# Performance work log

Hardware: AMD Instinct MI355X
Metric: run time of the kernel (lower is better)

## Reference

```python
import jax, jax.numpy as jnp
import numpy as np

T = 4            # number of atom types (experts)
F = (32, 64, 128)  # filter_neuron
H = (256, 256, 256)  # fitting_neuron
AXIS = 16        # axis_neuron
B, N, S = 8, 512, 128  # frames, atoms, SEL_A_max
DESC = AXIS * F[2]     # 2048, fitting input dim


def setup_inputs() -> dict:
    key = jax.random.key(0)
    ks = jax.random.split(key, 18)

    def w(k, shape, fan_in):
        return jax.random.normal(k, shape, jnp.float32) / np.float32(np.sqrt(fan_in))

    def b(k, shape):
        return 0.01 * jax.random.normal(k, shape, jnp.float32)

    return {
        "sym_coord": jax.random.normal(ks[0], (B, N, S, 4), jnp.float32),
        "types": jax.random.randint(ks[1], (B, N), 0, T, jnp.int32),
        # per-type filter MLP: 1 -> 32 -> 64 -> 128, tanh
        "Wf0": w(ks[2], (T, F[0], 1), 1), "bf0": b(ks[3], (T, F[0])),
        "Wf1": w(ks[4], (T, F[1], F[0]), F[0]), "bf1": b(ks[5], (T, F[1])),
        "Wf2": w(ks[6], (T, F[2], F[1]), F[1]), "bf2": b(ks[7], (T, F[2])),
        # per-type fitting MLP: 2048 -> 256 -> 256 -> 256 -> 1
        "Wt0": w(ks[8], (T, H[0], DESC), DESC), "bt0": b(ks[9], (T, H[0])),
        "Wt1": w(ks[10], (T, H[1], H[0]), H[0]), "bt1": b(ks[11], (T, H[1])),
        "Wt2": w(ks[12], (T, H[2], H[1]), H[1]), "bt2": b(ks[13], (T, H[2])),
        "Wo": w(ks[14], (T, 1, H[2]), H[2]), "bo": b(ks[15], (T, 1)),
    }


def reference(sym_coord, types, Wf0, bf0, Wf1, bf1, Wf2, bf2,
              Wt0, bt0, Wt1, bt1, Wt2, bt2, Wo, bo):
    t = types  # [B,N] expert index per atom
    s = sym_coord[..., :1]  # radial channel, [B,N,S,1]
    # type-routed filter MLP, vectorized via per-atom weight gather
    G = jnp.tanh(jnp.einsum('bnsi,bnfi->bnsf', s, Wf0[t]) + bf0[t][:, :, None, :])
    G = jnp.tanh(jnp.einsum('bnsf,bngf->bnsg', G, Wf1[t]) + bf1[t][:, :, None, :])
    G = jnp.tanh(jnp.einsum('bnsg,bnmg->bnsm', G, Wf2[t]) + bf2[t][:, :, None, :])  # [B,N,S,128]
    # RG = R^T G : [B,N,4,128]
    RG = jnp.einsum('bnsd,bnsm->bndm', sym_coord, G)
    # GRRG = RG^T RG[:, :AXIS] : [B,N,128,AXIS]
    GRRG = jnp.einsum('bndm,bnda->bnma', RG, RG[..., :AXIS])
    D = GRRG.reshape(GRRG.shape[0], GRRG.shape[1], -1)  # [B,N,2048]
    # type-routed fitting MLP
    h = jnp.tanh(jnp.einsum('bnd,bnhd->bnh', D, Wt0[t]) + bt0[t])
    h = jnp.tanh(jnp.einsum('bnh,bngh->bng', h, Wt1[t]) + bt1[t])
    h = jnp.tanh(jnp.einsum('bng,bnhg->bnh', h, Wt2[t]) + bt2[t])
    E_atom = jnp.einsum('bnh,bnoh->bno', h, Wo[t])[..., 0] + bo[t][..., 0]  # [B,N]
    return E_atom.sum(axis=-1)  # per-frame energy, [B]
```

## Files before the change

kernel.cpp:

```cpp
#include <hip/hip_runtime.h>
#include <hip/hip_bf16.h>

#define NATOMS 4096
#define DESC_ 2048
#define MAXTILES 67

typedef short short8 __attribute__((ext_vector_type(8)));
typedef float f32x4 __attribute__((ext_vector_type(4)));
typedef unsigned short u16x8 __attribute__((ext_vector_type(8)));
typedef unsigned short u16x4 __attribute__((ext_vector_type(4)));
typedef unsigned short u16;

__device__ __forceinline__ float fast_tanh(float x) {
    float e = __expf(2.0f * x);
    return 1.0f - 2.0f * __builtin_amdgcn_rcpf(e + 1.0f);
}

__device__ __forceinline__ float bf2f(u16 h) {
    union { unsigned int u; float f; } v; v.u = ((unsigned int)h) << 16;
    return v.f;
}
__device__ __forceinline__ void f2bf_split(float x, u16& hi, u16& lo) {
    union { float f; unsigned int u; } v; v.f = x;
    unsigned int hb = v.u & 0xffff0000u;
    hi = (u16)(hb >> 16);
    union { unsigned int u; float f; } w; w.u = hb;
    union { float f; unsigned int u; } z; z.f = x - w.f;
    lo = (u16)(z.u >> 16);
}

__device__ __forceinline__ void conv4(const float* __restrict__ src,
                                      u16* __restrict__ dh, u16* __restrict__ dl,
                                      int idx)
{
    float4 v = *(const float4*)(src + idx);
    u16x4 oh, ol;
    u16 h, l;
    f2bf_split(v.x, h, l); oh[0] = h; ol[0] = l;
    f2bf_split(v.y, h, l); oh[1] = h; ol[1] = l;
    f2bf_split(v.z, h, l); oh[2] = h; ol[2] = l;
    f2bf_split(v.w, h, l); oh[3] = h; ol[3] = l;
    *(u16x4*)(dh + idx) = oh;
    *(u16x4*)(dl + idx) = ol;
}

__global__ __launch_bounds__(256) void prep_kernel(
    const int* __restrict__ types, int* __restrict__ perm, int* __restrict__ meta,
    const float* __restrict__ Wf1, u16* __restrict__ F1h, u16* __restrict__ F1l,
    const float* __restrict__ Wf2, u16* __restrict__ F2h, u16* __restrict__ F2l,
    const float* __restrict__ Wt0, u16* __restrict__ W0h, u16* __restrict__ W0l,
    const float* __restrict__ Wt1, u16* __restrict__ W1h, u16* __restrict__ W1l,
    const float* __restrict__ Wt2, u16* __restrict__ W2h, u16* __restrict__ W2l)
{
    __shared__ int cnt[256 * 4];
    __shared__ int tot[4];
    __shared__ int tstart[4];
    int b = blockIdx.x;
    int tid = threadIdx.x;
    if (b == 0) {
        int base = tid * 16;
        int c0 = 0, c1 = 0, c2 = 0, c3 = 0;
        for (int i = 0; i < 16; ++i) {
            int t = types[base + i];
            c0 += (t == 0); c1 += (t == 1); c2 += (t == 2); c3 += (t == 3);
        }
        cnt[tid * 4 + 0] = c0; cnt[tid * 4 + 1] = c1;
        cnt[tid * 4 + 2] = c2; cnt[tid * 4 + 3] = c3;
        __syncthreads();
        if (tid < 4) {
            int run = 0;
            for (int th = 0; th < 256; ++th) {
                int v = cnt[th * 4 + tid];
                cnt[th * 4 + tid] = run;
                run += v;
            }
            tot[tid] = run;
        }
        __syncthreads();
        if (tid == 0) {
            int run = 0, nt = 0;
            for (int t = 0; t < 4; ++t) { tstart[t] = run; run += tot[t]; }
            for (int t = 0; t < 4; ++t) {
                int cT = tot[t];
                for (int off = 0; off < cT; off += 64) {
                    meta[1 + nt * 3 + 0] = t;
                    meta[1 + nt * 3 + 1] = tstart[t] + off;
                    meta[1 + nt * 3 + 2] = (cT - off < 64) ? (cT - off) : 64;
                    nt++;
                }
            }
            meta[0] = nt;
        }
        __syncthreads();
        for (int i = 0; i < 16; ++i) {
            int idx = base + i;
            int t = types[idx];
            perm[tstart[t] + cnt[tid * 4 + t]++] = idx;
        }
        return;
    }
    b -= 1;
    const float* src; u16 *dh, *dl; int n, base;
    if (b < 2048)      { src = Wt0; dh = W0h; dl = W0l; n = 2097152; base = b; }
    else if (b < 2304) { src = Wt1; dh = W1h; dl = W1l; n = 262144;  base = b - 2048; }
    else if (b < 2560) { src = Wt2; dh = W2h; dl = W2l; n = 262144;  base = b - 2304; }
    else if (b < 2568) { src = Wf1; dh = F1h; dl = F1l; n = 8192;    base = b - 2560; }
    else               { src = Wf2; dh = F2h; dl = F2l; n = 32768;   base = b - 2568; }
    int idx = (base * 256 + tid) * 4;
    if (idx < n) conv4(src, dh, dl, idx);
}

__global__ __launch_bounds__(256) void filter_kernel(
    const float* __restrict__ sym, const int* __restrict__ types,
    const int* __restrict__ perm,
    const float* __restrict__ Wf0, const float* __restrict__ bf0,
    const u16* __restrict__ F1h, const u16* __restrict__ F1l,
    const float* __restrict__ bf1,
    const u16* __restrict__ F2h, const u16* __restrict__ F2l,
    const float* __restrict__ bf2,
    u16* __restrict__ Dh, u16* __restrict__ Dl)
{
    __shared__ char lds[40960] __attribute__((aligned(16)));
    float* Rl  = (float*)lds;
    u16*   G1h = (u16*)(lds + 2048);
    u16*   G1l = (u16*)(lds + 20480);
    float* RGl = (float*)(lds + 38912);

    int p = blockIdx.x;
    int tid = threadIdx.x;
    int atom = perm[p];
    int t = __builtin_amdgcn_readfirstlane(types[atom]);
    int lane = tid & 63;
    int wv   = tid >> 6;
    int kg   = lane >> 4;
    int l15  = lane & 15;

    ((float2*)Rl)[tid] = ((const float2*)(sym + (size_t)atom * 512))[tid];

    {
        const float4* w0p = (const float4*)(Wf0 + t * 32 + kg * 8);
        float4 w04 = w0p[0], w14 = w0p[1];
        const float4* b0p = (const float4*)(bf0 + t * 32 + kg * 8);
        float4 b04 = b0p[0], b14 = b0p[1];

        short8 ah[2], al[2];
        #pragma unroll
        for (int mi = 0; mi < 2; ++mi) {
            int s = (wv * 2 + mi) * 16 + l15;
            float sv = sym[(size_t)atom * 512 + s * 4];
            float g[8];
            g[0] = fast_tanh(sv * w04.x + b04.x);
            g[1] = fast_tanh(sv * w04.y + b04.y);
            g[2] = fast_tanh(sv * w04.z + b04.z);
            g[3] = fast_tanh(sv * w04.w + b04.w);
            g[4] = fast_tanh(sv * w14.x + b14.x);
            g[5] = fast_tanh(sv * w14.y + b14.y);
            g[6] = fast_tanh(sv * w14.z + b14.z);
            g[7] = fast_tanh(sv * w14.w + b14.w);
            #pragma unroll
            for (int j = 0; j < 8; ++j) {
                u16 h, l; f2bf_split(g[j], h, l);
                ah[mi][j] = (short)h; al[mi][j] = (short)l;
            }
        }

        short8 b1h[4], b1l[4];
        float  bias1[4];
        #pragma unroll
        for (int nt = 0; nt < 4; ++nt) {
            int off = t * 2048 + (nt * 16 + l15) * 32 + kg * 8;
            b1h[nt] = *(const short8*)(F1h + off);
            b1l[nt] = *(const short8*)(F1l + off);
            bias1[nt] = bf1[t * 64 + nt * 16 + l15];
        }
        #pragma unroll
        for (int mi = 0; mi < 2; ++mi) {
            int mt = wv * 2 + mi;
            #pragma unroll
            for (int nt = 0; nt < 4; ++nt) {
                f32x4 acc = {0.f, 0.f, 0.f, 0.f};
                acc = __builtin_amdgcn_mfma_f32_16x16x32_bf16(ah[mi], b1h[nt], acc, 0, 0, 0);
                acc = __builtin_amdgcn_mfma_f32_16x16x32_bf16(ah[mi], b1l[nt], acc, 0, 0, 0);
                acc = __builtin_amdgcn_mfma_f32_16x16x32_bf16(al[mi], b1h[nt], acc, 0, 0, 0);
                int rowb = mt * 16 + kg * 4;
                #pragma unroll
                for (int r = 0; r < 4; ++r) {
                    u16 h, l;
                    f2bf_split(fast_tanh(acc[r] + bias1[nt]), h, l);
                    G1h[(rowb + r) * 72 + nt * 16 + l15] = h;
                    G1l[(rowb + r) * 72 + nt * 16 + l15] = l;
                }
            }
        }
    }
    __syncthreads();

    {
        short8 b2h[2][2], b2l[2][2];
        float  bias2[2];
        #pragma unroll
        for (int ntl = 0; ntl < 2; ++ntl) {
            int nt = wv * 2 + ntl;
            bias2[ntl] = bf2[t * 128 + nt * 16 + l15];
            #pragma unroll
            for (int ks = 0; ks < 2; ++ks) {
                int off = t * 8192 + (nt * 16 + l15) * 64 + ks * 32 + kg * 8;
                b2h[ntl][ks] = *(const short8*)(F2h + off);
                b2l[ntl][ks] = *(const short8*)(F2l + off);
            }
        }
        float rg[4][2];
        #pragma unroll
        for (int d = 0; d < 4; ++d) { rg[d][0] = 0.f; rg[d][1] = 0.f; }

        #pragma unroll 2
        for (int mt = 0; mt < 8; ++mt) {
            int i0 = (mt * 16 + l15) * 72 + kg * 8;
            short8 a0h = *(const short8*)&G1h[i0];
            short8 a0l = *(const short8*)&G1l[i0];
            short8 a1h = *(const short8*)&G1h[i0 + 32];
            short8 a1l = *(const short8*)&G1l[i0 + 32];
            f32x4 acc0 = {0.f,0.f,0.f,0.f}, acc1 = {0.f,0.f,0.f,0.f};
            acc0 = __builtin_amdgcn_mfma_f32_16x16x32_bf16(a0h, b2h[0][0], acc0, 0,0,0);
            acc0 = __builtin_amdgcn_mfma_f32_16x16x32_bf16(a0h, b2l[0][0], acc0, 0,0,0);
            acc0 = __builtin_amdgcn_mfma_f32_16x16x32_bf16(a0l, b2h[0][0], acc0, 0,0,0);
            acc0 = __builtin_amdgcn_mfma_f32_16x16x32_bf16(a1h, b2h[0][1], acc0, 0,0,0);
            acc0 = __builtin_amdgcn_mfma_f32_16x16x32_bf16(a1h, b2l[0][1], acc0, 0,0,0);
            acc0 = __builtin_amdgcn_mfma_f32_16x16x32_bf16(a1l, b2h[0][1], acc0, 0,0,0);
            acc1 = __builtin_amdgcn_mfma_f32_16x16x32_bf16(a0h, b2h[1][0], acc1, 0,0,0);
            acc1 = __builtin_amdgcn_mfma_f32_16x16x32_bf16(a0h, b2l[1][0], acc1, 0,0,0);
            acc1 = __builtin_amdgcn_mfma_f32_16x16x32_bf16(a0l, b2h[1][0], acc1, 0,0,0);
            acc1 = __builtin_amdgcn_mfma_f32_16x16x32_bf16(a1h, b2h[1][1], acc1, 0,0,0);
            acc1 = __builtin_amdgcn_mfma_f32_16x16x32_bf16(a1h, b2l[1][1], acc1, 0,0,0);
            acc1 = __builtin_amdgcn_mfma_f32_16x16x32_bf16(a1l, b2h[1][1], acc1, 0,0,0);
            int rowb = mt * 16 + kg * 4;
            #pragma unroll
            for (int r = 0; r < 4; ++r) {
                float4 R4 = *(const float4*)&Rl[(rowb + r) * 4];
                float g0 = fast_tanh(acc0[r] + bias2[0]);
                float g1 = fast_tanh(acc1[r] + bias2[1]);
                rg[0][0] += R4.x * g0; rg[1][0] += R4.y * g0;
                rg[2][0] += R4.z * g0; rg[3][0] += R4.w * g0;
                rg[0][1] += R4.x * g1; rg[1][1] += R4.y * g1;
                rg[2][1] += R4.z * g1; rg[3][1] += R4.w * g1;
            }
        }
        #pragma unroll
        for (int off = 16; off < 64; off <<= 1) {
            #pragma unroll
            for (int d = 0; d < 4; ++d) {
                rg[d][0] += __shfl_xor(rg[d][0], off, 64);
                rg[d][1] += __shfl_xor(rg[d][1], off, 64);
            }
        }
        if (kg == 0) {
            #pragma unroll
            for (int d = 0; d < 4; ++d) {
                RGl[d * 128 + wv * 32 + l15]      = rg[d][0];
                RGl[d * 128 + wv * 32 + 16 + l15] = rg[d][1];
            }
        }
    }
    __syncthreads();

    {
        int m = tid >> 1;
        int ab = (tid & 1) * 8;
        float rm0 = RGl[0 * 128 + m], rm1 = RGl[1 * 128 + m];
        float rm2 = RGl[2 * 128 + m], rm3 = RGl[3 * 128 + m];
        u16x8 oh, ol;
        #pragma unroll
        for (int q = 0; q < 8; ++q) {
            int a = ab + q;
            float v = rm0 * RGl[0 * 128 + a] + rm1 * RGl[1 * 128 + a]
                    + rm2 * RGl[2 * 128 + a] + rm3 * RGl[3 * 128 + a];
            u16 h, l; f2bf_split(v, h, l);
            oh[q] = h; ol[q] = l;
        }
        size_t base = (size_t)p * DESC_ + m * 16 + ab;
        *(u16x8*)(Dh + base) = oh;
        *(u16x8*)(Dl + base) = ol;
    }
}

__global__ __launch_bounds__(256) void fit0_partial(
    const u16* __restrict__ inh, const u16* __restrict__ inl,
    const u16* __restrict__ Wh,  const u16* __restrict__ Wl,
    float* __restrict__ part, const int* __restrict__ meta)
{
    __shared__ char lds[18432] __attribute__((aligned(16)));
    u16* Ath = (u16*)lds;
    u16* Atl = (u16*)(lds + 9216);

    int ntiles = meta[0];
    int b = blockIdx.x;
    int tile = b >> 4;
    if (tile >= ntiles) return;
    int hq  = (b >> 2) & 3;
    int ksp = b & 3;
    int t   = __builtin_amdgcn_readfirstlane(meta[1 + tile * 3 + 0]);
    int p0  = meta[1 + tile * 3 + 1];
    int cnt = meta[1 + tile * 3 + 2];
    int h0b = hq * 64;

    int tid = threadIdx.x;
    int lane = tid & 63;
    int wv   = tid >> 6;
    int kg   = lane >> 4;
    int l15  = lane & 15;

    int srow = tid >> 2;
    int skc  = (tid & 3) * 16;
    int agrow = p0 + srow; if (agrow > NATOMS - 1) agrow = NATOMS - 1;
    const u16* arow_h = inh + (size_t)agrow * 2048;
    const u16* arow_l = inl + (size_t)agrow * 2048;
    int hmy = h0b + wv * 16 + l15;
    const u16* brow_h = Wh + ((size_t)t * 256 + hmy) * 2048;
    const u16* brow_l = Wl + ((size_t)t * 256 + hmy) * 2048;

    f32x4 acc[4];
    #pragma unroll
    for (int mt = 0; mt < 4; ++mt) acc[mt] = (f32x4){0.f, 0.f, 0.f, 0.f};

    int kbase = ksp * 512;
    for (int k0 = kbase; k0 < kbase + 512; k0 += 64) {
        u16x8 a0 = *(const u16x8*)(arow_h + k0 + skc);
        u16x8 a1 = *(const u16x8*)(arow_h + k0 + skc + 8);
        u16x8 a2 = *(const u16x8*)(arow_l + k0 + skc);
        u16x8 a3 = *(const u16x8*)(arow_l + k0 + skc + 8);
        __syncthreads();
        int si = srow * 72 + skc;
        *(u16x8*)&Ath[si]     = a0;
        *(u16x8*)&Ath[si + 8] = a1;
        *(u16x8*)&Atl[si]     = a2;
        *(u16x8*)&Atl[si + 8] = a3;
        __syncthreads();

        #pragma unroll
        for (int ks = 0; ks < 2; ++ks) {
            short8 bh = *(const short8*)(brow_h + k0 + ks * 32 + kg * 8);
            short8 bl = *(const short8*)(brow_l + k0 + ks * 32 + kg * 8);
            #pragma unroll
            for (int mt = 0; mt < 4; ++mt) {
                int ai = (mt * 16 + l15) * 72 + ks * 32 + kg * 8;
                short8 ah = *(const short8*)&Ath[ai];
                short8 al = *(const short8*)&Atl[ai];
                acc[mt] = __builtin_amdgcn_mfma_f32_16x16x32_bf16(ah, bh, acc[mt], 0, 0, 0);
                acc[mt] = __builtin_amdgcn_mfma_f32_16x16x32_bf16(ah, bl, acc[mt], 0, 0, 0);
                acc[mt] = __builtin_amdgcn_mfma_f32_16x16x32_bf16(al, bh, acc[mt], 0, 0, 0);
            }
        }
    }

    float* pdst = part + (size_t)ksp * (NATOMS * 256);
    #pragma unroll
    for (int mt = 0; mt < 4; ++mt) {
        #pragma unroll
        for (int r = 0; r < 4; ++r) {
            int al = mt * 16 + kg * 4 + r;
            if (al < cnt)
                pdst[(size_t)(p0 + al) * 256 + hmy] = acc[mt][r];
        }
    }
}

__global__ __launch_bounds__(256) void fit0_epi(
    const float* __restrict__ part, const float* __restrict__ bias,
    const int* __restrict__ perm, const int* __restrict__ types,
    u16* __restrict__ outh, u16* __restrict__ outl)
{
    const int PN = NATOMS * 256;
    int idx = (blockIdx.x * 256 + threadIdx.x) * 4;
    if (idx >= PN) return;
    int p = idx >> 8;
    int t = types[perm[p]];
    float4 s0 = *(const float4*)(part + idx);
    float4 s1 = *(const float4*)(part + PN + idx);
    float4 s2 = *(const float4*)(part + 2 * PN + idx);
    float4 s3 = *(const float4*)(part + 3 * PN + idx);
    float4 bv = *(const float4*)(bias + t * 256 + (idx & 255));
    float v0 = fast_tanh(s0.x + s1.x + s2.x + s3.x + bv.x);
    float v1 = fast_tanh(s0.y + s1.y + s2.y + s3.y + bv.y);
    float v2 = fast_tanh(s0.z + s1.z + s2.z + s3.z + bv.z);
    float v3 = fast_tanh(s0.w + s1.w + s2.w + s3.w + bv.w);
    u16x4 oh, ol; u16 h, l;
    f2bf_split(v0, h, l); oh[0] = h; ol[0] = l;
    f2bf_split(v1, h, l); oh[1] = h; ol[1] = l;
    f2bf_split(v2, h, l); oh[2] = h; ol[2] = l;
    f2bf_split(v3, h, l); oh[3] = h; ol[3] = l;
    *(u16x4*)(outh + idx) = oh;
    *(u16x4*)(outl + idx) = ol;
}

__global__ __launch_bounds__(256) void fit_mfma(
    const u16* __restrict__ inh, const u16* __restrict__ inl,
    const u16* __restrict__ Wh,  const u16* __restrict__ Wl,
    const float* __restrict__ bias,
    u16* __restrict__ outh, u16* __restrict__ outl,
    int K, const int* __restrict__ meta)
{
    __shared__ char lds[36864] __attribute__((aligned(16)));
    u16* Ath = (u16*)lds;
    u16* Atl = (u16*)(lds + 9216);
    u16* Bth = (u16*)(lds + 18432);
    u16* Btl = (u16*)(lds + 27648);

    int ntiles = meta[0];
    int tile = blockIdx.x >> 2;
    if (tile >= ntiles) return;
    int hq  = blockIdx.x & 3;
    int t   = __builtin_amdgcn_readfirstlane(meta[1 + tile * 3 + 0]);
    int p0  = meta[1 + tile * 3 + 1];
    int cnt = meta[1 + tile * 3 + 2];
    int h0b = hq * 64;

    int tid = threadIdx.x;
    int lane = tid & 63;
    int wv   = tid >> 6;
    int kg   = lane >> 4;
    int l15  = lane & 15;

    int srow = tid >> 2;
    int skc  = (tid & 3) * 16;
    int agrow = p0 + srow; if (agrow > NATOMS - 1) agrow = NATOMS - 1;
    const u16* arow_h = inh + (size_t)agrow * K;
    const u16* arow_l = inl + (size_t)agrow * K;
    const u16* brow_h = Wh + ((size_t)t * 256 + h0b + srow) * K;
    const u16* brow_l = Wl + ((size_t)t * 256 + h0b + srow) * K;

    f32x4 acc[4];
    #pragma unroll
    for (int mt = 0; mt < 4; ++mt) acc[mt] = (f32x4){0.f, 0.f, 0.f, 0.f};

    for (int k0 = 0; k0 < K; k0 += 64) {
        u16x8 a0 = *(const u16x8*)(arow_h + k0 + skc);
        u16x8 a1 = *(const u16x8*)(arow_h + k0 + skc + 8);
        u16x8 a2 = *(const u16x8*)(arow_l + k0 + skc);
        u16x8 a3 = *(const u16x8*)(arow_l + k0 + skc + 8);
        u16x8 b0 = *(const u16x8*)(brow_h + k0 + skc);
        u16x8 b1 = *(const u16x8*)(brow_h + k0 + skc + 8);
        u16x8 b2 = *(const u16x8*)(brow_l + k0 + skc);
        u16x8 b3 = *(const u16x8*)(brow_l + k0 + skc + 8);
        __syncthreads();
        int si = srow * 72 + skc;
        *(u16x8*)&Ath[si]     = a0;
        *(u16x8*)&Ath[si + 8] = a1;
        *(u16x8*)&Atl[si]     = a2;
        *(u16x8*)&Atl[si + 8] = a3;
        *(u16x8*)&Bth[si]     = b0;
        *(u16x8*)&Bth[si + 8] = b1;
        *(u16x8*)&Btl[si]     = b2;
        *(u16x8*)&Btl[si + 8] = b3;
        __syncthreads();

        #pragma unroll
        for (int ks = 0; ks < 2; ++ks) {
            int bi = (wv * 16 + l15) * 72 + ks * 32 + kg * 8;
            short8 bh = *(const short8*)&Bth[bi];
            short8 bl = *(const short8*)&Btl[bi];
            #pragma unroll
            for (int mt = 0; mt < 4; ++mt) {
                int ai = (mt * 16 + l15) * 72 + ks * 32 + kg * 8;
                short8 ah = *(const short8*)&Ath[ai];
                short8 al = *(const short8*)&Atl[ai];
                acc[mt] = __builtin_amdgcn_mfma_f32_16x16x32_bf16(ah, bh, acc[mt], 0, 0, 0);
                acc[mt] = __builtin_amdgcn_mfma_f32_16x16x32_bf16(ah, bl, acc[mt], 0, 0, 0);
                acc[mt] = __builtin_amdgcn_mfma_f32_16x16x32_bf16(al, bh, acc[mt], 0, 0, 0);
            }
        }
    }

    int h = h0b + wv * 16 + l15;
    float b = bias[t * 256 + h];
    #pragma unroll
    for (int mt = 0; mt < 4; ++mt) {
        #pragma unroll
        for (int r = 0; r < 4; ++r) {
            int al = mt * 16 + kg * 4 + r;
            if (al < cnt) {
                float v = fast_tanh(acc[mt][r] + b);
                u16 hh, ll; f2bf_split(v, hh, ll);
                size_t o = (size_t)(p0 + al) * 256 + h;
                outh[o] = hh;
                outl[o] = ll;
            }
        }
    }
}

__global__ __launch_bounds__(256) void final_kernel(
    const u16* __restrict__ h2h, const u16* __restrict__ h2l,
    const int* __restrict__ perm, const int* __restrict__ types,
    const float* __restrict__ Wo, const float* __restrict__ bo,
    float* __restrict__ e2)
{
    int tid = threadIdx.x;
    int wv = tid >> 6;
    int lane = tid & 63;
    int p = blockIdx.x * 4 + wv;
    int atom = perm[p];
    int t = types[atom];
    const u16* hh = h2h + (size_t)p * 256;
    const u16* hl = h2l + (size_t)p * 256;
    float e = 0.f;
    #pragma unroll
    for (int r = 0; r < 4; ++r) {
        int h = r * 64 + lane;
        e += (bf2f(hh[h]) + bf2f(hl[h])) * Wo[t * 256 + h];
    }
    #pragma unroll
    for (int off = 32; off > 0; off >>= 1)
        e += __shfl_xor(e, off, 64);
    if (lane == 0) e2[atom] = e + bo[t];
}

__global__ __launch_bounds__(256) void reduce_kernel(
    const float* __restrict__ e2, float* __restrict__ out)
{
    __shared__ float s[256];
    int b = blockIdx.x;
    int tid = threadIdx.x;
    s[tid] = e2[b * 512 + tid] + e2[b * 512 + 256 + tid];
    __syncthreads();
    #pragma unroll
    for (int off = 128; off > 0; off >>= 1) {
        if (tid < off) s[tid] += s[tid + off];
        __syncthreads();
    }
    if (tid == 0) out[b] = s[0];
}

extern "C" void kernel_launch(void* const* d_in, const int* in_sizes, int n_in,
                              void* d_out, int out_size, void* d_ws, size_t ws_size,
                              hipStream_t stream) {
    const float* sym = (const float*)d_in[0];
    const int*   types = (const int*)d_in[1];
    const float* Wf0 = (const float*)d_in[2];
    const float* bf0 = (const float*)d_in[3];
    const float* Wf1 = (const float*)d_in[4];
    const float* bf1 = (const float*)d_in[5];
    const float* Wf2 = (const float*)d_in[6];
    const float* bf2 = (const float*)d_in[7];
    const float* Wt0 = (const float*)d_in[8];
    const float* bt0 = (const float*)d_in[9];
    const float* Wt1 = (const float*)d_in[10];
    const float* bt1 = (const float*)d_in[11];
    const float* Wt2 = (const float*)d_in[12];
    const float* bt2 = (const float*)d_in[13];
    const float* Wo  = (const float*)d_in[14];
    const float* bo  = (const float*)d_in[15];
    float* out = (float*)d_out;

    char* ws = (char*)d_ws;
    const size_t MB = 1024 * 1024;
    int*  meta = (int*)ws;
    int*  perm = (int*)(ws + 1024);
    char* base = ws + 32768;
    u16*  Dh   = (u16*)(base);
    u16*  Dl   = (u16*)(base + 16 * MB);
    u16*  h1h  = (u16*)(base);
    u16*  h1l  = (u16*)(base + 2 * MB);
    u16*  h2h  = (u16*)(base + 4 * MB);
    u16*  h2l  = (u16*)(base + 6 * MB);
    float* e2  = (float*)(base + 8 * MB);
    u16*  h0h  = (u16*)(base + 32 * MB);
    u16*  h0l  = (u16*)(base + 34 * MB);
    u16*  W0h  = (u16*)(base + 36 * MB);
    u16*  W0l  = (u16*)(base + 40 * MB);
    u16*  W1h  = (u16*)(base + 44 * MB);
    u16*  W1l  = (u16*)(base + 44 * MB + 512 * 1024);
    u16*  W2h  = (u16*)(base + 45 * MB);
    u16*  W2l  = (u16*)(base + 45 * MB + 512 * 1024);
    u16*  F1h  = (u16*)(base + 46 * MB);
    u16*  F1l  = (u16*)(base + 46 * MB + 16 * 1024);
    u16*  F2h  = (u16*)(base + 46 * MB + 32 * 1024);
    u16*  F2l  = (u16*)(base + 46 * MB + 96 * 1024);
    float* part = (float*)(base + 47 * MB);

    prep_kernel<<<2601, 256, 0, stream>>>(types, perm, meta,
                                          Wf1, F1h, F1l, Wf2, F2h, F2l,
                                          Wt0, W0h, W0l, Wt1, W1h, W1l,
                                          Wt2, W2h, W2l);

    filter_kernel<<<NATOMS, 256, 0, stream>>>(sym, types, perm,
                                              Wf0, bf0, F1h, F1l, bf1,
                                              F2h, F2l, bf2, Dh, Dl);

    fit0_partial<<<MAXTILES * 16, 256, 0, stream>>>(Dh, Dl, W0h, W0l, part, meta);
    fit0_epi<<<NATOMS / 4, 256, 0, stream>>>(part, bt0, perm, types, h0h, h0l);

    fit_mfma<<<MAXTILES * 4, 256, 0, stream>>>(h0h, h0l, W1h, W1l, bt1,
                                               h1h, h1l, 256, meta);
    fit_mfma<<<MAXTILES * 4, 256, 0, stream>>>(h1h, h1l, W2h, W2l, bt2,
                                               h2h, h2l, 256, meta);

    final_kernel<<<NATOMS / 4, 256, 0, stream>>>(h2h, h2l, perm, types, Wo, bo, e2);
    reduce_kernel<<<8, 256, 0, stream>>>(e2, out);
}
```

Before: 137.5 us.

## Split filter kernel into two row halves to halve LDS and raise occupancy

The filter kernel now processes the 128 neighbor rows in two passes of 64, reusing a half-size LDS buffer for the first hidden layer. The shared allocation drops from about 40 KB to 22 KB, and launch bounds request 8 blocks per CU, so more blocks can be resident at once. In exchange the layer-2 weights are reloaded once per pass, there is an extra barrier per pass, and there is less instruction-level parallelism per wave, since one accumulator chain replaces two.

```diff
diff --git a/kernel.cpp b/kernel.cpp
--- a/kernel.cpp
+++ b/kernel.cpp
@@ -110,7 +110,7 @@
     if (idx < n) conv4(src, dh, dl, idx);
 }
 
-__global__ __launch_bounds__(256) void filter_kernel(
+__global__ __launch_bounds__(256, 8) void filter_kernel(
     const float* __restrict__ sym, const int* __restrict__ types,
     const int* __restrict__ perm,
     const float* __restrict__ Wf0, const float* __restrict__ bf0,
@@ -120,11 +120,11 @@
     const float* __restrict__ bf2,
     u16* __restrict__ Dh, u16* __restrict__ Dl)
 {
-    __shared__ char lds[40960] __attribute__((aligned(16)));
+    __shared__ char lds[22528] __attribute__((aligned(16)));
     float* Rl  = (float*)lds;
     u16*   G1h = (u16*)(lds + 2048);
-    u16*   G1l = (u16*)(lds + 20480);
-    float* RGl = (float*)(lds + 38912);
+    u16*   G1l = (u16*)(lds + 11264);
+    float* RGl = (float*)(lds + 20480);
 
     int p = blockIdx.x;
     int tid = threadIdx.x;
@@ -137,16 +137,19 @@
 
     ((float2*)Rl)[tid] = ((const float2*)(sym + (size_t)atom * 512))[tid];
 
-    {
-        const float4* w0p = (const float4*)(Wf0 + t * 32 + kg * 8);
-        float4 w04 = w0p[0], w14 = w0p[1];
-        const float4* b0p = (const float4*)(bf0 + t * 32 + kg * 8);
-        float4 b04 = b0p[0], b14 = b0p[1];
-
-        short8 ah[2], al[2];
-        #pragma unroll
-        for (int mi = 0; mi < 2; ++mi) {
-            int s = (wv * 2 + mi) * 16 + l15;
+    float rg[4][2];
+    #pragma unroll
+    for (int d = 0; d < 4; ++d) { rg[d][0] = 0.f; rg[d][1] = 0.f; }
+
+    #pragma unroll 1
+    for (int half = 0; half < 2; ++half) {
+        short8 ah, al;
+        {
+            const float4* w0p = (const float4*)(Wf0 + t * 32 + kg * 8);
+            float4 w04 = w0p[0], w14 = w0p[1];
+            const float4* b0p = (const float4*)(bf0 + t * 32 + kg * 8);
+            float4 b04 = b0p[0], b14 = b0p[1];
+            int s = half * 64 + wv * 16 + l15;
             float sv = sym[(size_t)atom * 512 + s * 4];
             float g[8];
             g[0] = fast_tanh(sv * w04.x + b04.x);
@@ -160,105 +163,80 @@
             #pragma unroll
             for (int j = 0; j < 8; ++j) {
                 u16 h, l; f2bf_split(g[j], h, l);
-                ah[mi][j] = (short)h; al[mi][j] = (short)l;
-            }
-        }
-
-        short8 b1h[4], b1l[4];
-        float  bias1[4];
+                ah[j] = (short)h; al[j] = (short)l;
+            }
+        }
+
         #pragma unroll
         for (int nt = 0; nt < 4; ++nt) {
             int off = t * 2048 + (nt * 16 + l15) * 32 + kg * 8;
-            b1h[nt] = *(const short8*)(F1h + off);
-            b1l[nt] = *(const short8*)(F1l + off);
-            bias1[nt] = bf1[t * 64 + nt * 16 + l15];
-        }
-        #pragma unroll
-        for (int mi = 0; mi < 2; ++mi) {
-            int mt = wv * 2 + mi;
+            short8 b1h = *(const short8*)(F1h + off);
+            short8 b1l = *(const short8*)(F1l + off);
+            float bias1 = bf1[t * 64 + nt * 16 + l15];
+            f32x4 acc = {0.f, 0.f, 0.f, 0.f};
+            acc = __builtin_amdgcn_mfma_f32_16x16x32_bf16(ah, b1h, acc, 0, 0, 0);
+            acc = __builtin_amdgcn_mfma_f32_16x16x32_bf16(ah, b1l, acc, 0, 0, 0);
+            acc = __builtin_amdgcn_mfma_f32_16x16x32_bf16(al, b1h, acc, 0, 0, 0);
+            int rowb = wv * 16 + kg * 4;
             #pragma unroll
-            for (int nt = 0; nt < 4; ++nt) {
+            for (int r = 0; r < 4; ++r) {
+                u16 h, l;
+                f2bf_split(fast_tanh(acc[r] + bias1), h, l);
+                G1h[(rowb + r) * 72 + nt * 16 + l15] = h;
+                G1l[(rowb + r) * 72 + nt * 16 + l15] = l;
+            }
+        }
+        __syncthreads();
+
+        #pragma unroll
+        for (int ntl = 0; ntl < 2; ++ntl) {
+            int nt = wv * 2 + ntl;
+            float bias2 = bf2[t * 128 + nt * 16 + l15];
+            int off0 = t * 8192 + (nt * 16 + l15) * 64 + kg * 8;
+            short8 b2h0 = *(const short8*)(F2h + off0);
+            short8 b2l0 = *(const short8*)(F2l + off0);
+            short8 b2h1 = *(const short8*)(F2h + off0 + 32);
+            short8 b2l1 = *(const short8*)(F2l + off0 + 32);
+            #pragma unroll
+            for (int lt = 0; lt < 4; ++lt) {
+                int i0 = (lt * 16 + l15) * 72 + kg * 8;
+                short8 a0h = *(const short8*)&G1h[i0];
+                short8 a0l = *(const short8*)&G1l[i0];
+                short8 a1h = *(const short8*)&G1h[i0 + 32];
+                short8 a1l = *(const short8*)&G1l[i0 + 32];
                 f32x4 acc = {0.f, 0.f, 0.f, 0.f};
-                acc = __builtin_amdgcn_mfma_f32_16x16x32_bf16(ah[mi], b1h[nt], acc, 0, 0, 0);
-                acc = __builtin_amdgcn_mfma_f32_16x16x32_bf16(ah[mi], b1l[nt], acc, 0, 0, 0);
-                acc = __builtin_amdgcn_mfma_f32_16x16x32_bf16(al[mi], b1h[nt], acc, 0, 0, 0);
-                int rowb = mt * 16 + kg * 4;
+                acc = __builtin_amdgcn_mfma_f32_16x16x32_bf16(a0h, b2h0, acc, 0, 0, 0);
+                acc = __builtin_amdgcn_mfma_f32_16x16x32_bf16(a0h, b2l0, acc, 0, 0, 0);
+                acc = __builtin_amdgcn_mfma_f32_16x16x32_bf16(a0l, b2h0, acc, 0, 0, 0);
+                acc = __builtin_amdgcn_mfma_f32_16x16x32_bf16(a1h, b2h1, acc, 0, 0, 0);
+                acc = __builtin_amdgcn_mfma_f32_16x16x32_bf16(a1h, b2l1, acc, 0, 0, 0);
+                acc = __builtin_amdgcn_mfma_f32_16x16x32_bf16(a1l, b2h1, acc, 0, 0, 0);
+                int rowb = half * 64 + lt * 16 + kg * 4;
                 #pragma unroll
                 for (int r = 0; r < 4; ++r) {
-                    u16 h, l;
-                    f2bf_split(fast_tanh(acc[r] + bias1[nt]), h, l);
-                    G1h[(rowb + r) * 72 + nt * 16 + l15] = h;
-                    G1l[(rowb + r) * 72 + nt * 16 + l15] = l;
+                    float4 R4 = *(const float4*)&Rl[(rowb + r) * 4];
+                    float g = fast_tanh(acc[r] + bias2);
+                    rg[0][ntl] += R4.x * g; rg[1][ntl] += R4.y * g;
+                    rg[2][ntl] += R4.z * g; rg[3][ntl] += R4.w * g;
                 }
             }
         }
-    }
-    __syncthreads();
-
-    {
-        short8 b2h[2][2], b2l[2][2];
-        float  bias2[2];
-        #pragma unroll
-        for (int ntl = 0; ntl < 2; ++ntl) {
-            int nt = wv * 2 + ntl;
-            bias2[ntl] = bf2[t * 128 + nt * 16 + l15];
-            #pragma unroll
-            for (int ks = 0; ks < 2; ++ks) {
-                int off = t * 8192 + (nt * 16 + l15) * 64 + ks * 32 + kg * 8;
-                b2h[ntl][ks] = *(const short8*)(F2h + off);
-                b2l[ntl][ks] = *(const short8*)(F2l + off);
-            }
-        }
-        float rg[4][2];
-        #pragma unroll
-        for (int d = 0; d < 4; ++d) { rg[d][0] = 0.f; rg[d][1] = 0.f; }
-
-        #pragma unroll 2
-        for (int mt = 0; mt < 8; ++mt) {
-            int i0 = (mt * 16 + l15) * 72 + kg * 8;
-            short8 a0h = *(const short8*)&G1h[i0];
-            short8 a0l = *(const short8*)&G1l[i0];
-            short8 a1h = *(const short8*)&G1h[i0 + 32];
-            short8 a1l = *(const short8*)&G1l[i0 + 32];
-            f32x4 acc0 = {0.f,0.f,0.f,0.f}, acc1 = {0.f,0.f,0.f,0.f};
-            acc0 = __builtin_amdgcn_mfma_f32_16x16x32_bf16(a0h, b2h[0][0], acc0, 0,0,0);
-            acc0 = __builtin_amdgcn_mfma_f32_16x16x32_bf16(a0h, b2l[0][0], acc0, 0,0,0);
-            acc0 = __builtin_amdgcn_mfma_f32_16x16x32_bf16(a0l, b2h[0][0], acc0, 0,0,0);
-            acc0 = __builtin_amdgcn_mfma_f32_16x16x32_bf16(a1h, b2h[0][1], acc0, 0,0,0);
-            acc0 = __builtin_amdgcn_mfma_f32_16x16x32_bf16(a1h, b2l[0][1], acc0, 0,0,0);
-            acc0 = __builtin_amdgcn_mfma_f32_16x16x32_bf16(a1l, b2h[0][1], acc0, 0,0,0);
-            acc1 = __builtin_amdgcn_mfma_f32_16x16x32_bf16(a0h, b2h[1][0], acc1, 0,0,0);
-            acc1 = __builtin_amdgcn_mfma_f32_16x16x32_bf16(a0h, b2l[1][0], acc1, 0,0,0);
-            acc1 = __builtin_amdgcn_mfma_f32_16x16x32_bf16(a0l, b2h[1][0], acc1, 0,0,0);
-            acc1 = __builtin_amdgcn_mfma_f32_16x16x32_bf16(a1h, b2h[1][1], acc1, 0,0,0);
-            acc1 = __builtin_amdgcn_mfma_f32_16x16x32_bf16(a1h, b2l[1][1], acc1, 0,0,0);
-            acc1 = __builtin_amdgcn_mfma_f32_16x16x32_bf16(a1l, b2h[1][1], acc1, 0,0,0);
-            int rowb = mt * 16 + kg * 4;
-            #pragma unroll
-            for (int r = 0; r < 4; ++r) {
-                float4 R4 = *(const float4*)&Rl[(rowb + r) * 4];
-                float g0 = fast_tanh(acc0[r] + bias2[0]);
-                float g1 = fast_tanh(acc1[r] + bias2[1]);
-                rg[0][0] += R4.x * g0; rg[1][0] += R4.y * g0;
-                rg[2][0] += R4.z * g0; rg[3][0] += R4.w * g0;
-                rg[0][1] += R4.x * g1; rg[1][1] += R4.y * g1;
-                rg[2][1] += R4.z * g1; rg[3][1] += R4.w * g1;
-            }
-        }
-        #pragma unroll
-        for (int off = 16; off < 64; off <<= 1) {
-            #pragma unroll
-            for (int d = 0; d < 4; ++d) {
-                rg[d][0] += __shfl_xor(rg[d][0], off, 64);
-                rg[d][1] += __shfl_xor(rg[d][1], off, 64);
-            }
-        }
-        if (kg == 0) {
-            #pragma unroll
-            for (int d = 0; d < 4; ++d) {
-                RGl[d * 128 + wv * 32 + l15]      = rg[d][0];
-                RGl[d * 128 + wv * 32 + 16 + l15] = rg[d][1];
-            }
+        __syncthreads();
+    }
+
+    #pragma unroll
+    for (int off = 16; off < 64; off <<= 1) {
+        #pragma unroll
+        for (int d = 0; d < 4; ++d) {
+            rg[d][0] += __shfl_xor(rg[d][0], off, 64);
+            rg[d][1] += __shfl_xor(rg[d][1], off, 64);
+        }
+    }
+    if (kg == 0) {
+        #pragma unroll
+        for (int d = 0; d < 4; ++d) {
+            RGl[d * 128 + wv * 32 + l15]      = rg[d][0];
+            RGl[d * 128 + wv * 32 + 16 + l15] = rg[d][1];
         }
     }
     __syncthreads();
```

Result: slower. 151.0 us (+9.8%).
